# Optimization experiments

Measured on AMD Instinct MI355X. Metric: run time of the kernel, lower is better.

The kernel has to match this reference:

```python
import jax, jax.numpy as jnp
import numpy as np

B, S, DIM, H = 2, 2048, 1024, 16
DK = DIM // H  # 64
NEG = -10000000000.0


def setup_inputs() -> dict:
    key = jax.random.key(0)
    k1, k2, k3, k4, k5, k6 = jax.random.split(key, 6)
    dec_xs = jax.random.normal(k1, (B, S, DIM), dtype=jnp.float32)
    enc_xs = jax.random.normal(k2, (B, S, DIM), dtype=jnp.float32)
    mask = jax.random.randint(k3, (B, S, S), 0, 2, dtype=jnp.int32)
    # torch Linear weights: out = x @ W.T, bias=False
    sc = 1.0 / np.sqrt(DIM)
    Wq = jax.random.normal(k4, (DIM, DIM), dtype=jnp.float32) * sc
    Wkv = jax.random.normal(k5, (2 * DIM, DIM), dtype=jnp.float32) * sc
    Wo = jax.random.normal(k6, (DIM, DIM), dtype=jnp.float32) * sc
    return {"dec_xs": dec_xs, "enc_xs": enc_xs, "Wq": Wq, "Wkv": Wkv, "Wo": Wo, "mask": mask}


def reference(dec_xs, enc_xs, Wq, Wkv, Wo, mask):
    b, s, dim = enc_xs.shape
    qs = dec_xs @ Wq.T                      # [b,s,dim]  (dropout inactive in eval)
    kv = enc_xs @ Wkv.T                     # [b,s,2*dim]
    ks, vs = jnp.split(kv, 2, axis=-1)
    # head layout: view(b, s, dk, h) -- heads LAST, as in the original
    qs = qs.reshape(b, s, DK, H)
    ks = ks.reshape(b, s, DK, H)
    vs = vs.reshape(b, s, DK, H)
    scores = jnp.einsum('bqdh,bkdh->bqkh', qs, ks) / np.sqrt(DK)
    scores = jnp.where(mask[..., None] == 0, NEG, scores)
    weights = jax.nn.softmax(scores, axis=-2)  # softmax over key axis
    out = jnp.einsum('bqkh,bkdh->bqdh', weights, vs).reshape(b, s, dim)
    return out @ Wo.T
```

## Files before the change

kernel.cpp:

```cpp
#include <hip/hip_runtime.h>
#include <hip/hip_bf16.h>

#define BB 2
#define SS 2048
#define DIMM 1024
#define HH 16
#define DKK 64
#define QSCALE 0.18033688011112042592f

using bf16 = __hip_bfloat16;
typedef __attribute__((ext_vector_type(8))) short v8s;
typedef __attribute__((ext_vector_type(4))) short v4s;
typedef __attribute__((ext_vector_type(4))) float f32x4;

__device__ __forceinline__ void cvt4(const float* __restrict__ s,
                                     bf16* __restrict__ d, int idx) {
  const float4 f = ((const float4*)s)[idx];
  bf16 t[4] = {__float2bfloat16(f.x), __float2bfloat16(f.y),
               __float2bfloat16(f.z), __float2bfloat16(f.w)};
  *(v4s*)(d + (size_t)idx * 4) = *(const v4s*)t;
}

__global__ __launch_bounds__(256) void convert_pack_kernel(
    const float* __restrict__ dec, const float* __restrict__ enc,
    const float* __restrict__ Wq, const float* __restrict__ Wkv,
    const float* __restrict__ Wo, const int* __restrict__ mask,
    bf16* __restrict__ decb, bf16* __restrict__ encb, bf16* __restrict__ Wqb,
    bf16* __restrict__ Wkvb, bf16* __restrict__ Wob,
    unsigned long long* __restrict__ mp) {
  const int gid = blockIdx.x * 256 + threadIdx.x;
  const int NT = 256 * 1024;
#pragma unroll
  for (int i = 0; i < 4; ++i) cvt4(dec, decb, gid + i * NT);
#pragma unroll
  for (int i = 0; i < 4; ++i) cvt4(enc, encb, gid + i * NT);
  cvt4(Wq, Wqb, gid);
#pragma unroll
  for (int i = 0; i < 2; ++i) cvt4(Wkv, Wkvb, gid + i * NT);
  {
    const int n = gid >> 8;
    const int c4 = (gid & 255) * 4;
    const int h = c4 >> 6, d0 = c4 & 63;
    const float* src = Wo + (size_t)n * DIMM + h;
    bf16 t[4];
#pragma unroll
    for (int i2 = 0; i2 < 4; ++i2)
      t[i2] = __float2bfloat16(src[(d0 + i2) * 16]);
    *(v4s*)(Wob + (size_t)n * DIMM + c4) = *(const v4s*)t;
  }
  const int lane = threadIdx.x & 63;
  const int wave_id = gid >> 6;
  for (int i = 0; i < 32; ++i) {
    const size_t w = (size_t)wave_id * 32 + i;
    const unsigned long long bm = __ballot(mask[w * 64 + lane] != 0);
    if (lane == 0) mp[w] = bm;
  }
}

__global__ __launch_bounds__(256) void proj_gemm_kernel(
    const bf16* __restrict__ decb, const bf16* __restrict__ encb,
    const bf16* __restrict__ Wqb, const bf16* __restrict__ Wkvb,
    bf16* __restrict__ Qr, bf16* __restrict__ Kr, bf16* __restrict__ Vt) {
  __shared__ __align__(16) bf16 As[128][72];
  __shared__ __align__(16) bf16 Bs[128][72];
  const int t = threadIdx.x;
  const int wave = t >> 6, lane = t & 63;
  const int quad = lane >> 4, l15 = lane & 15;
  const int wm = (wave >> 1) * 64, wn = (wave & 1) * 64;
  const int bx = blockIdx.x;
  const int kind = bx >> 3;
  const int g = bx & 7;
  const int m0 = blockIdx.y * 128;

  const int sr = t >> 2;
  const int sc = (t & 3) * 16;
  const int voff = (kind == 2) ? DIMM : 0;
  const int wr0 = sr * 16 + g * 2 + voff;
  const int wr1 = sr * 16 + g * 2 + 1 + voff;

  const bf16* arow0;
  const bf16* arow1;
  const bf16* brow0;
  const bf16* brow1;
  if (kind == 0) {
    arow0 = decb + (size_t)(m0 + sr) * DIMM;
    arow1 = decb + (size_t)(m0 + sr + 64) * DIMM;
    brow0 = Wqb + (size_t)wr0 * DIMM;
    brow1 = Wqb + (size_t)wr1 * DIMM;
  } else if (kind == 1) {
    arow0 = encb + (size_t)(m0 + sr) * DIMM;
    arow1 = encb + (size_t)(m0 + sr + 64) * DIMM;
    brow0 = Wkvb + (size_t)wr0 * DIMM;
    brow1 = Wkvb + (size_t)wr1 * DIMM;
  } else {
    arow0 = Wkvb + (size_t)wr0 * DIMM;
    arow1 = Wkvb + (size_t)wr1 * DIMM;
    brow0 = encb + (size_t)(m0 + sr) * DIMM;
    brow1 = encb + (size_t)(m0 + sr + 64) * DIMM;
  }

  v8s apf[4], bpf[4];
  auto loadAB = [&](int kc) {
    apf[0] = ((const v8s*)(arow0 + kc + sc))[0];
    apf[1] = ((const v8s*)(arow0 + kc + sc))[1];
    apf[2] = ((const v8s*)(arow1 + kc + sc))[0];
    apf[3] = ((const v8s*)(arow1 + kc + sc))[1];
    bpf[0] = ((const v8s*)(brow0 + kc + sc))[0];
    bpf[1] = ((const v8s*)(brow0 + kc + sc))[1];
    bpf[2] = ((const v8s*)(brow1 + kc + sc))[0];
    bpf[3] = ((const v8s*)(brow1 + kc + sc))[1];
  };

  f32x4 acc[4][4] = {};
  loadAB(0);

  for (int kc = 0; kc < DIMM; kc += 64) {
    __syncthreads();
    *(v8s*)&As[sr][sc] = apf[0];
    *(v8s*)&As[sr][sc + 8] = apf[1];
    *(v8s*)&As[sr + 64][sc] = apf[2];
    *(v8s*)&As[sr + 64][sc + 8] = apf[3];
    *(v8s*)&Bs[sr][sc] = bpf[0];
    *(v8s*)&Bs[sr][sc + 8] = bpf[1];
    *(v8s*)&Bs[sr + 64][sc] = bpf[2];
    *(v8s*)&Bs[sr + 64][sc + 8] = bpf[3];
    if (kc + 64 < DIMM) loadAB(kc + 64);
    __syncthreads();
#pragma unroll
    for (int ks = 0; ks < 2; ++ks) {
      v8s af[4], bfr[4];
#pragma unroll
      for (int i = 0; i < 4; ++i)
        af[i] = *(const v8s*)&As[wm + i * 16 + l15][ks * 32 + quad * 8];
#pragma unroll
      for (int j = 0; j < 4; ++j)
        bfr[j] = *(const v8s*)&Bs[wn + j * 16 + l15][ks * 32 + quad * 8];
#pragma unroll
      for (int i = 0; i < 4; ++i)
#pragma unroll
        for (int j = 0; j < 4; ++j)
          acc[i][j] = __builtin_amdgcn_mfma_f32_16x16x32_bf16(
              af[i], bfr[j], acc[i][j], 0, 0, 0);
    }
  }

#pragma unroll
  for (int i = 0; i < 4; ++i) {
#pragma unroll
    for (int r = 0; r < 4; ++r) {
      const int mm = wm + i * 16 + quad * 4 + r;
#pragma unroll
      for (int j = 0; j < 4; ++j) {
        const int nn = wn + j * 16 + l15;
        const float v = acc[i][j][r];
        if (kind == 0) {
          Qr[(size_t)(m0 + mm) * DIMM + g * 128 + nn] =
              __float2bfloat16(v * QSCALE);
        } else if (kind == 1) {
          Kr[(size_t)(m0 + mm) * DIMM + g * 128 + nn] = __float2bfloat16(v);
        } else {
          const int h = g * 2 + (mm >> 6), d = mm & 63;
          const int sn = m0 + nn;
          const int b = sn >> 11, s = sn & (SS - 1);
          Vt[(((size_t)b * HH + h) * DKK + d) * SS + s] = __float2bfloat16(v);
        }
      }
    }
  }
}

__global__ __launch_bounds__(256) void out_gemm_kernel(
    const bf16* __restrict__ A, const bf16* __restrict__ W,
    float* __restrict__ out) {
  __shared__ __align__(16) bf16 As[128][72];
  __shared__ __align__(16) bf16 Bs[64][72];
  const int t = threadIdx.x;
  const int wave = t >> 6, lane = t & 63;
  const int quad = lane >> 4, l15 = lane & 15;
  const int wm = (wave >> 1) * 64, wn = (wave & 1) * 32;
  const int n0 = blockIdx.x * 64;
  const int m0 = blockIdx.y * 128;
  const int sr = t >> 2;
  const int sc = (t & 3) * 16;

  v8s ar[4], br[2];
  auto loadA = [&](int kc) {
#pragma unroll
    for (int rr = 0; rr < 2; ++rr) {
      const bf16* p = A + (size_t)(m0 + sr + rr * 64) * DIMM + kc + sc;
#pragma unroll
      for (int i = 0; i < 2; ++i) ar[rr * 2 + i] = ((const v8s*)p)[i];
    }
  };
  auto loadB = [&](int kc) {
    const bf16* p = W + (size_t)(n0 + sr) * DIMM + kc + sc;
#pragma unroll
    for (int i = 0; i < 2; ++i) br[i] = ((const v8s*)p)[i];
  };

  f32x4 acc[4][2] = {};
  loadA(0);
  loadB(0);
  for (int kc = 0; kc < DIMM; kc += 64) {
    __syncthreads();
#pragma unroll
    for (int rr = 0; rr < 2; ++rr) {
      *(v8s*)&As[sr + rr * 64][sc] = ar[rr * 2 + 0];
      *(v8s*)&As[sr + rr * 64][sc + 8] = ar[rr * 2 + 1];
    }
    *(v8s*)&Bs[sr][sc] = br[0];
    *(v8s*)&Bs[sr][sc + 8] = br[1];
    if (kc + 64 < DIMM) {
      loadA(kc + 64);
      loadB(kc + 64);
    }
    __syncthreads();
#pragma unroll
    for (int ks = 0; ks < 2; ++ks) {
      v8s af[4], bfr[2];
#pragma unroll
      for (int i = 0; i < 4; ++i)
        af[i] = *(const v8s*)&As[wm + i * 16 + l15][ks * 32 + quad * 8];
#pragma unroll
      for (int j = 0; j < 2; ++j)
        bfr[j] = *(const v8s*)&Bs[wn + j * 16 + l15][ks * 32 + quad * 8];
#pragma unroll
      for (int i = 0; i < 4; ++i)
#pragma unroll
        for (int j = 0; j < 2; ++j)
          acc[i][j] = __builtin_amdgcn_mfma_f32_16x16x32_bf16(
              af[i], bfr[j], acc[i][j], 0, 0, 0);
    }
  }

#pragma unroll
  for (int i = 0; i < 4; ++i) {
#pragma unroll
    for (int r = 0; r < 4; ++r) {
      const int m = m0 + wm + i * 16 + quad * 4 + r;
#pragma unroll
      for (int j = 0; j < 2; ++j) {
        const int n = n0 + wn + j * 16 + l15;
        out[(size_t)m * DIMM + n] = acc[i][j][r];
      }
    }
  }
}

__global__ __launch_bounds__(256) void attn_kernel(
    const bf16* __restrict__ Qr, const bf16* __restrict__ Kr,
    const bf16* __restrict__ Vt, const unsigned long long* __restrict__ mp,
    bf16* __restrict__ Ar) {
  __shared__ __align__(16) bf16 Ks[2][64][72];
  __shared__ __align__(16) bf16 Vs[2][64][72];
  __shared__ __align__(16) bf16 Ps[4][32][72];

  const int t = threadIdx.x;
  const int wave = t >> 6, lane = t & 63;
  const int quad = lane >> 4, l15 = lane & 15;

  const int bx = blockIdx.x;
  const int xcd = bx & 7, j = bx >> 3;
  const int g = (xcd << 2) | (j & 3);
  const int tile = j >> 2;
  const int h = g & 15, b = g >> 4;

  const int qw = tile * 128 + wave * 32;
  const size_t bhv = ((size_t)b * HH + h) * DKK;

  v8s aq[2][2];
#pragma unroll
  for (int qf = 0; qf < 2; ++qf) {
    const bf16* qrow =
        Qr + ((size_t)(b * SS + qw + qf * 16 + l15)) * DIMM + h * 64;
    aq[qf][0] = *(const v8s*)(qrow + quad * 8);
    aq[qf][1] = *(const v8s*)(qrow + 32 + quad * 8);
  }

  f32x4 o[2][4] = {};
  float lsum[2][4] = {};

  const int r0 = t >> 2;
  const int c0 = (t & 3) * 16;

  auto loadK = [&](int kt, v8s* kr) {
    const bf16* p =
        Kr + ((size_t)(b * SS + kt * 64 + r0)) * DIMM + h * 64 + c0;
    kr[0] = ((const v8s*)p)[0];
    kr[1] = ((const v8s*)p)[1];
  };
  auto loadV = [&](int kt, v8s* vr) {
    const bf16* p = Vt + (bhv + r0) * SS + kt * 64 + c0;
    vr[0] = ((const v8s*)p)[0];
    vr[1] = ((const v8s*)p)[1];
  };

  v8s kreg[2], vreg[2];
  loadK(0, kreg);
  loadV(0, vreg);
  *(v8s*)&Ks[0][r0][c0] = kreg[0];
  *(v8s*)&Ks[0][r0][c0 + 8] = kreg[1];
  *(v8s*)&Vs[0][r0][c0] = vreg[0];
  *(v8s*)&Vs[0][r0][c0 + 8] = vreg[1];
  loadK(1, kreg);
  loadV(1, vreg);

  int p = 0;
  for (int kt = 0; kt < 32; ++kt) {
    __syncthreads();
    if (kt < 31) {
      *(v8s*)&Ks[p ^ 1][r0][c0] = kreg[0];
      *(v8s*)&Ks[p ^ 1][r0][c0 + 8] = kreg[1];
      *(v8s*)&Vs[p ^ 1][r0][c0] = vreg[0];
      *(v8s*)&Vs[p ^ 1][r0][c0 + 8] = vreg[1];
      if (kt < 30) {
        loadK(kt + 2, kreg);
        loadV(kt + 2, vreg);
      }
    }

    unsigned long long mw[2][4];
#pragma unroll
    for (int qf = 0; qf < 2; ++qf)
#pragma unroll
      for (int r = 0; r < 4; ++r)
        mw[qf][r] =
            mp[((size_t)b * SS + qw + qf * 16 + quad * 4 + r) * 32 + kt] >>
            l15;

    f32x4 sc[2][4];
#pragma unroll
    for (int n = 0; n < 4; ++n) {
      const v8s bk0 = *(const v8s*)&Ks[p][n * 16 + l15][quad * 8];
      const v8s bk1 = *(const v8s*)&Ks[p][n * 16 + l15][32 + quad * 8];
#pragma unroll
      for (int qf = 0; qf < 2; ++qf) {
        f32x4 z = {0.f, 0.f, 0.f, 0.f};
        z = __builtin_amdgcn_mfma_f32_16x16x32_bf16(aq[qf][0], bk0, z, 0, 0,
                                                    0);
        sc[qf][n] = __builtin_amdgcn_mfma_f32_16x16x32_bf16(aq[qf][1], bk1, z,
                                                            0, 0, 0);
      }
    }

#pragma unroll
    for (int qf = 0; qf < 2; ++qf)
#pragma unroll
      for (int n = 0; n < 4; ++n)
#pragma unroll
        for (int r = 0; r < 4; ++r) {
          const bool keep = (mw[qf][r] >> (n * 16)) & 1ULL;
          const float pw = keep ? __builtin_amdgcn_exp2f(sc[qf][n][r]) : 0.f;
          sc[qf][n][r] = pw;
          lsum[qf][r] += pw;
        }

#pragma unroll
    for (int qf = 0; qf < 2; ++qf)
#pragma unroll
      for (int n = 0; n < 4; ++n)
#pragma unroll
        for (int r = 0; r < 4; ++r)
          Ps[wave][qf * 16 + quad * 4 + r][n * 16 + l15] =
              __float2bfloat16(sc[qf][n][r]);

    v8s ap[2][2];
#pragma unroll
    for (int qf = 0; qf < 2; ++qf) {
      ap[qf][0] = *(const v8s*)&Ps[wave][qf * 16 + l15][quad * 8];
      ap[qf][1] = *(const v8s*)&Ps[wave][qf * 16 + l15][32 + quad * 8];
    }

#pragma unroll
    for (int n = 0; n < 4; ++n) {
      const v8s bv0 = *(const v8s*)&Vs[p][n * 16 + l15][quad * 8];
      const v8s bv1 = *(const v8s*)&Vs[p][n * 16 + l15][32 + quad * 8];
#pragma unroll
      for (int qf = 0; qf < 2; ++qf) {
        o[qf][n] = __builtin_amdgcn_mfma_f32_16x16x32_bf16(ap[qf][0], bv0,
                                                           o[qf][n], 0, 0, 0);
        o[qf][n] = __builtin_amdgcn_mfma_f32_16x16x32_bf16(ap[qf][1], bv1,
                                                           o[qf][n], 0, 0, 0);
      }
    }
    p ^= 1;
  }

#pragma unroll
  for (int qf = 0; qf < 2; ++qf)
#pragma unroll
    for (int r = 0; r < 4; ++r) {
      float l = lsum[qf][r];
      l += __shfl_xor(l, 1);
      l += __shfl_xor(l, 2);
      l += __shfl_xor(l, 4);
      l += __shfl_xor(l, 8);
      const float inv = 1.f / l;
      const size_t row = (size_t)b * SS + qw + qf * 16 + quad * 4 + r;
#pragma unroll
      for (int n = 0; n < 4; ++n) {
        Ar[row * DIMM + h * 64 + n * 16 + l15] =
            __float2bfloat16(o[qf][n][r] * inv);
      }
    }
}

extern "C" void kernel_launch(void* const* d_in, const int* in_sizes, int n_in,
                              void* d_out, int out_size, void* d_ws,
                              size_t ws_size, hipStream_t stream) {
  const float* dec = (const float*)d_in[0];
  const float* enc = (const float*)d_in[1];
  const float* Wq = (const float*)d_in[2];
  const float* Wkv = (const float*)d_in[3];
  const float* Wo = (const float*)d_in[4];
  const int* mask = (const int*)d_in[5];
  float* out = (float*)d_out;

  bf16* decb = (bf16*)d_out;
  bf16* Wqb = (bf16*)((char*)d_out + ((size_t)2 * SS * DIMM * 2));

  char* ws = (char*)d_ws;
  size_t off = 0;
  bf16* encb = (bf16*)(ws + off);
  bf16* Ar = (bf16*)(ws + off);   off += (size_t)2 * SS * DIMM * 2;
  bf16* Wkvb = (bf16*)(ws + off); off += (size_t)2 * DIMM * DIMM * 2;
  bf16* Wob = (bf16*)(ws + off);  off += (size_t)DIMM * DIMM * 2;
  bf16* Qr = (bf16*)(ws + off);   off += (size_t)2 * SS * DIMM * 2;
  bf16* Kr = (bf16*)(ws + off);   off += (size_t)2 * SS * DIMM * 2;
  bf16* Vt = (bf16*)(ws + off);   off += (size_t)2 * SS * DIMM * 2;
  unsigned long long* mp = (unsigned long long*)(ws + off);

  dim3 blk(256);
  convert_pack_kernel<<<dim3(1024), blk, 0, stream>>>(
      dec, enc, Wq, Wkv, Wo, mask, decb, encb, Wqb, Wkvb, Wob, mp);
  proj_gemm_kernel<<<dim3(24, 32), blk, 0, stream>>>(decb, encb, Wqb, Wkvb, Qr,
                                                     Kr, Vt);
  attn_kernel<<<dim3(512), dim3(256), 0, stream>>>(Qr, Kr, Vt, mp, Ar);
  out_gemm_kernel<<<dim3(16, 32), blk, 0, stream>>>(Ar, Wob, out);
}
```

Measured before the change: 247.2 us.

## Switch attention to 32x32 MFMA with register-resident P and ones-column row sums

Rewrites the attention inner loop to use 32x32x16 bf16 MFMA, computing S^T so the probability tile stays in registers and is rearranged with permlane32 swaps instead of going through an LDS round-trip. Row sums come from an extra MFMA against a ones vector rather than per-lane accumulation and shuffles. The packed mask is transposed to a [b][kchunk][q] layout so each lane loads one coalesced word per tile, with the next tile's mask prefetched. This adds a third MFMA per k-slice and relies on gfx950-specific instructions (cvt_pk_bf16, permlane32_swap).

```diff
diff --git a/kernel.cpp b/kernel.cpp
--- a/kernel.cpp
+++ b/kernel.cpp
@@ -12,6 +12,7 @@
 typedef __attribute__((ext_vector_type(8))) short v8s;
 typedef __attribute__((ext_vector_type(4))) short v4s;
 typedef __attribute__((ext_vector_type(4))) float f32x4;
+typedef __attribute__((ext_vector_type(16))) float f32x16;
 
 __device__ __forceinline__ void cvt4(const float* __restrict__ s,
                                      bf16* __restrict__ d, int idx) {
@@ -19,6 +20,12 @@
   bf16 t[4] = {__float2bfloat16(f.x), __float2bfloat16(f.y),
                __float2bfloat16(f.z), __float2bfloat16(f.w)};
   *(v4s*)(d + (size_t)idx * 4) = *(const v4s*)t;
+}
+
+__device__ __forceinline__ int cvt_pk_bf16(float lo, float hi) {
+  int r;
+  asm("v_cvt_pk_bf16_f32 %0, %1, %2" : "=v"(r) : "v"(lo), "v"(hi));
+  return r;
 }
 
 __global__ __launch_bounds__(256) void convert_pack_kernel(
@@ -53,7 +60,12 @@
   for (int i = 0; i < 32; ++i) {
     const size_t w = (size_t)wave_id * 32 + i;
     const unsigned long long bm = __ballot(mask[w * 64 + lane] != 0);
-    if (lane == 0) mp[w] = bm;
+    if (lane == 0) {
+      const int bb = (int)(w >> 16);
+      const int qq = (int)((w >> 5) & 2047);
+      const int kc = (int)(w & 31);
+      mp[((size_t)bb * 32 + kc) * SS + qq] = bm;
+    }
   }
 }
 
@@ -253,39 +265,40 @@
     bf16* __restrict__ Ar) {
   __shared__ __align__(16) bf16 Ks[2][64][72];
   __shared__ __align__(16) bf16 Vs[2][64][72];
-  __shared__ __align__(16) bf16 Ps[4][32][72];
 
   const int t = threadIdx.x;
   const int wave = t >> 6, lane = t & 63;
-  const int quad = lane >> 4, l15 = lane & 15;
+  const int l31 = lane & 31, hf = lane >> 5;
 
   const int bx = blockIdx.x;
   const int xcd = bx & 7, j = bx >> 3;
   const int g = (xcd << 2) | (j & 3);
   const int tile = j >> 2;
-  const int h = g & 15, b = g >> 4;
+  const int hd = g & 15, b = g >> 4;
 
   const int qw = tile * 128 + wave * 32;
-  const size_t bhv = ((size_t)b * HH + h) * DKK;
-
-  v8s aq[2][2];
-#pragma unroll
-  for (int qf = 0; qf < 2; ++qf) {
-    const bf16* qrow =
-        Qr + ((size_t)(b * SS + qw + qf * 16 + l15)) * DIMM + h * 64;
-    aq[qf][0] = *(const v8s*)(qrow + quad * 8);
-    aq[qf][1] = *(const v8s*)(qrow + 32 + quad * 8);
-  }
-
-  f32x4 o[2][4] = {};
-  float lsum[2][4] = {};
+  const size_t bhv = ((size_t)b * HH + hd) * DKK;
+
+  v8s bq[4];
+  {
+    const bf16* qrow = Qr + ((size_t)(b * SS + qw + l31)) * DIMM + hd * 64;
+#pragma unroll
+    for (int cs = 0; cs < 4; ++cs)
+      bq[cs] = *(const v8s*)(qrow + cs * 16 + 8 * hf);
+  }
+
+  v8s vones;
+#pragma unroll
+  for (int i = 0; i < 8; ++i) vones[i] = (short)0x3F80;
+
+  f32x16 o0 = {}, o1 = {}, ol = {};
 
   const int r0 = t >> 2;
   const int c0 = (t & 3) * 16;
 
   auto loadK = [&](int kt, v8s* kr) {
     const bf16* p =
-        Kr + ((size_t)(b * SS + kt * 64 + r0)) * DIMM + h * 64 + c0;
+        Kr + ((size_t)(b * SS + kt * 64 + r0)) * DIMM + hd * 64 + c0;
     kr[0] = ((const v8s*)p)[0];
     kr[1] = ((const v8s*)p)[1];
   };
@@ -293,6 +306,9 @@
     const bf16* p = Vt + (bhv + r0) * SS + kt * 64 + c0;
     vr[0] = ((const v8s*)p)[0];
     vr[1] = ((const v8s*)p)[1];
+  };
+  auto loadM = [&](int kt) {
+    return mp[((size_t)b * 32 + kt) * SS + qw + l31];
   };
 
   v8s kreg[2], vreg[2];
@@ -304,6 +320,7 @@
   *(v8s*)&Vs[0][r0][c0 + 8] = vreg[1];
   loadK(1, kreg);
   loadV(1, vreg);
+  unsigned long long mwcur = loadM(0);
 
   int p = 0;
   for (int kt = 0; kt < 32; ++kt) {
@@ -318,91 +335,74 @@
         loadV(kt + 2, vreg);
       }
     }
-
-    unsigned long long mw[2][4];
-#pragma unroll
-    for (int qf = 0; qf < 2; ++qf)
-#pragma unroll
-      for (int r = 0; r < 4; ++r)
-        mw[qf][r] =
-            mp[((size_t)b * SS + qw + qf * 16 + quad * 4 + r) * 32 + kt] >>
-            l15;
-
-    f32x4 sc[2][4];
-#pragma unroll
-    for (int n = 0; n < 4; ++n) {
-      const v8s bk0 = *(const v8s*)&Ks[p][n * 16 + l15][quad * 8];
-      const v8s bk1 = *(const v8s*)&Ks[p][n * 16 + l15][32 + quad * 8];
-#pragma unroll
-      for (int qf = 0; qf < 2; ++qf) {
-        f32x4 z = {0.f, 0.f, 0.f, 0.f};
-        z = __builtin_amdgcn_mfma_f32_16x16x32_bf16(aq[qf][0], bk0, z, 0, 0,
-                                                    0);
-        sc[qf][n] = __builtin_amdgcn_mfma_f32_16x16x32_bf16(aq[qf][1], bk1, z,
-                                                            0, 0, 0);
+    unsigned long long mwnext = (kt < 31) ? loadM(kt + 1) : 0ULL;
+    const unsigned long long mq = mwcur >> (4 * hf);
+
+    f32x16 st[2];
+#pragma unroll
+    for (int n = 0; n < 2; ++n) {
+      f32x16 s = {};
+#pragma unroll
+      for (int cs = 0; cs < 4; ++cs) {
+        const v8s ak = *(const v8s*)&Ks[p][n * 32 + l31][cs * 16 + 8 * hf];
+        s = __builtin_amdgcn_mfma_f32_32x32x16_bf16(ak, bq[cs], s, 0, 0, 0);
       }
-    }
-
-#pragma unroll
-    for (int qf = 0; qf < 2; ++qf)
-#pragma unroll
-      for (int n = 0; n < 4; ++n)
-#pragma unroll
-        for (int r = 0; r < 4; ++r) {
-          const bool keep = (mw[qf][r] >> (n * 16)) & 1ULL;
-          const float pw = keep ? __builtin_amdgcn_exp2f(sc[qf][n][r]) : 0.f;
-          sc[qf][n][r] = pw;
-          lsum[qf][r] += pw;
+      st[n] = s;
+    }
+
+    int pd[8][2];
+#pragma unroll
+    for (int n = 0; n < 2; ++n)
+#pragma unroll
+      for (int g2 = 0; g2 < 4; ++g2)
+#pragma unroll
+        for (int jj = 0; jj < 2; ++jj) {
+          const int bp = 32 * n + 8 * g2 + 2 * jj;
+          const int m = g2 * 4 + 2 * jj;
+          const float p0 = ((mq >> bp) & 1)
+                               ? __builtin_amdgcn_exp2f(st[n][m])
+                               : 0.f;
+          const float p1 = ((mq >> (bp + 1)) & 1)
+                               ? __builtin_amdgcn_exp2f(st[n][m + 1])
+                               : 0.f;
+          pd[n * 4 + g2][jj] = cvt_pk_bf16(p0, p1);
         }
 
-#pragma unroll
-    for (int qf = 0; qf < 2; ++qf)
-#pragma unroll
-      for (int n = 0; n < 4; ++n)
-#pragma unroll
-        for (int r = 0; r < 4; ++r)
-          Ps[wave][qf * 16 + quad * 4 + r][n * 16 + l15] =
-              __float2bfloat16(sc[qf][n][r]);
-
-    v8s ap[2][2];
-#pragma unroll
-    for (int qf = 0; qf < 2; ++qf) {
-      ap[qf][0] = *(const v8s*)&Ps[wave][qf * 16 + l15][quad * 8];
-      ap[qf][1] = *(const v8s*)&Ps[wave][qf * 16 + l15][32 + quad * 8];
-    }
-
-#pragma unroll
-    for (int n = 0; n < 4; ++n) {
-      const v8s bv0 = *(const v8s*)&Vs[p][n * 16 + l15][quad * 8];
-      const v8s bv1 = *(const v8s*)&Vs[p][n * 16 + l15][32 + quad * 8];
-#pragma unroll
-      for (int qf = 0; qf < 2; ++qf) {
-        o[qf][n] = __builtin_amdgcn_mfma_f32_16x16x32_bf16(ap[qf][0], bv0,
-                                                           o[qf][n], 0, 0, 0);
-        o[qf][n] = __builtin_amdgcn_mfma_f32_16x16x32_bf16(ap[qf][1], bv1,
-                                                           o[qf][n], 0, 0, 0);
-      }
-    }
+    v8s af[4];
+#pragma unroll
+    for (int ks = 0; ks < 4; ++ks) {
+      int a0 = pd[2 * ks][0], b0 = pd[2 * ks + 1][0];
+      int a1 = pd[2 * ks][1], b1 = pd[2 * ks + 1][1];
+      asm("v_permlane32_swap_b32 %0, %1" : "+v"(a0), "+v"(b0));
+      asm("v_permlane32_swap_b32 %0, %1" : "+v"(a1), "+v"(b1));
+      int4 w;
+      w.x = a0;
+      w.y = a1;
+      w.z = b0;
+      w.w = b1;
+      af[ks] = *(v8s*)&w;
+    }
+
+#pragma unroll
+    for (int ks = 0; ks < 4; ++ks) {
+      const v8s bv0 = *(const v8s*)&Vs[p][l31][ks * 16 + 8 * hf];
+      const v8s bv1 = *(const v8s*)&Vs[p][32 + l31][ks * 16 + 8 * hf];
+      o0 = __builtin_amdgcn_mfma_f32_32x32x16_bf16(af[ks], bv0, o0, 0, 0, 0);
+      o1 = __builtin_amdgcn_mfma_f32_32x32x16_bf16(af[ks], bv1, o1, 0, 0, 0);
+      ol = __builtin_amdgcn_mfma_f32_32x32x16_bf16(af[ks], vones, ol, 0, 0, 0);
+    }
+    mwcur = mwnext;
     p ^= 1;
   }
 
 #pragma unroll
-  for (int qf = 0; qf < 2; ++qf)
-#pragma unroll
-    for (int r = 0; r < 4; ++r) {
-      float l = lsum[qf][r];
-      l += __shfl_xor(l, 1);
-      l += __shfl_xor(l, 2);
-      l += __shfl_xor(l, 4);
-      l += __shfl_xor(l, 8);
-      const float inv = 1.f / l;
-      const size_t row = (size_t)b * SS + qw + qf * 16 + quad * 4 + r;
-#pragma unroll
-      for (int n = 0; n < 4; ++n) {
-        Ar[row * DIMM + h * 64 + n * 16 + l15] =
-            __float2bfloat16(o[qf][n][r] * inv);
-      }
-    }
+  for (int m = 0; m < 16; ++m) {
+    const float inv = __builtin_amdgcn_rcpf(ol[m]);
+    const int q = qw + (m & 3) + 8 * (m >> 2) + 4 * hf;
+    const size_t row = (size_t)b * SS + q;
+    Ar[row * DIMM + hd * 64 + l31] = __float2bfloat16(o0[m] * inv);
+    Ar[row * DIMM + hd * 64 + 32 + l31] = __float2bfloat16(o1[m] * inv);
+  }
 }
 
 extern "C" void kernel_launch(void* const* d_in, const int* in_sizes, int n_in,
```

Result: no change. 245.2 us (-0.8%).
